# Kernel tuning notes

Hardware: AMD Instinct MI355X
Metric: run time of the kernel (lower is better)

## Reference

```python
import jax, jax.numpy as jnp
import numpy as np

L, C_IN, C, C_OUT, M, H, W = 4, 3, 64, 1, 64, 512, 512
INV_SQRT2 = 0.7071067811865476  # complex normal: re/im parts have variance 1/2


def setup_inputs() -> dict:
    key = jax.random.key(0)
    ks = jax.random.split(key, 12)

    def unif(k, shape, fan_in):
        lim = 1.0 / np.sqrt(fan_in)
        return jax.random.uniform(k, shape, jnp.float32, -lim, lim)

    return {
        "u": jax.random.normal(ks[0], (1, H, W), jnp.float32),
        "x": jax.random.normal(ks[1], (2, H, W), jnp.float32),
        "enc_w": unif(ks[2], (C, C_IN), C_IN),
        "enc_b": unif(ks[3], (C,), C_IN),
        "dec_w": unif(ks[4], (C_OUT, C), C),
        "dec_b": unif(ks[5], (C_OUT,), C),
        "conv1_w": unif(ks[6], (L, C, C), C),
        "conv1_b": unif(ks[7], (L, C), C),
        "conv2_w": unif(ks[8], (L, C, C), C),
        "conv2_b": unif(ks[9], (L, C), C),
        "A_re": jax.random.normal(ks[10], (L, C, C, M, M), jnp.float32) * INV_SQRT2,
        "A_im": jax.random.normal(ks[11], (L, C, C, M, M), jnp.float32) * INV_SQRT2,
    }


def pconv(w, b, v):
    # 1x1 conv == channel matmul: w [o,i], v [i,h,w]
    return jnp.einsum('oi,ihw->ohw', w, v) + b[:, None, None]


def spectral_conv(v, A):
    # v: [C, H, W] real; A: [C, C, M, M] complex
    Cv, Hv, Wv = v.shape
    c = jnp.fft.rfft2(v, norm='forward')[:, :, :M]      # truncate last axis -> [C, H, M]
    c = jnp.roll(c, M // 2, axis=1)[:, :M]              # center + truncate rows -> [C, M, M]
    c = jnp.einsum('oimn,imn->omn', A, c)               # per-mode channel mixing
    c = jnp.pad(c, ((0, 0), (0, Hv - M), (0, Wv // 2 + 1 - M)))
    c = jnp.roll(c, -(M // 2), axis=1)
    return jnp.fft.irfft2(c, s=(Hv, Wv), norm='forward')


def reference(u, x, enc_w, enc_b, dec_w, dec_b, conv1_w, conv1_b, conv2_w, conv2_b, A_re, A_im):
    A = A_re + 1j * A_im                                 # [L, C, C, M, M]
    v = jnp.concatenate([x, u], 0)                       # [C_IN, H, W]
    v = pconv(enc_w, enc_b, v)                           # [C, H, W]
    for l in range(A.shape[0]):
        s = spectral_conv(v, A[l])
        v = v + jax.nn.gelu(pconv(conv2_w[l], conv2_b[l], jax.nn.gelu(pconv(conv1_w[l], conv1_b[l], s))))
    return pconv(dec_w, dec_b, v)                        # [C_OUT, H, W]
```

## Files before the change

### kernel.cpp

```cpp
#include <hip/hip_runtime.h>


constexpr int Hn = 512, Wn = 512, Cn = 64, Mn = 64, Ln = 4;
constexpr int HWn = Hn * Wn;

typedef _Float16 half8 __attribute__((ext_vector_type(8)));
typedef float f32x4 __attribute__((ext_vector_type(4)));

__device__ __forceinline__ float gelu_f(float x) {
  float t = 0.7978845608028654f * (x + 0.044715f * x * x * x);
  float e = __expf(2.0f * t);
  float th = 1.0f - 2.0f / (e + 1.0f);
  return 0.5f * x * (1.0f + th);
}

__global__ __launch_bounds__(256) void k_init_tw(_Float16* __restrict__ B1t,
                                                 _Float16* __restrict__ A2t,
                                                 _Float16* __restrict__ A3t,
                                                 _Float16* __restrict__ B4t) {
  int j = blockIdx.x * 256 + threadIdx.x;
  const float TPI = 6.283185307179586f / 512.0f;
  {
    int n = j >> 9, w = j & 511;
    int idx = ((n & 63) * w) & 511;
    float ang = TPI * (float)idx;
    B1t[j] = (_Float16)((n < 64) ? cosf(ang) : -sinf(ang));
  }
  {
    int mp = j >> 9, h = j & 511;
    int idx = (((mp & 63) - 32) * h) & 511;
    float ang = TPI * (float)idx;
    A2t[j] = (_Float16)((mp < 64) ? cosf(ang) : -sinf(ang));
  }
  {
    int h = j >> 7, k = j & 127;
    int idx = (((k & 63) - 32) * h) & 511;
    float ang = TPI * (float)idx;
    A3t[j] = (_Float16)((k < 64) ? cosf(ang) : sinf(ang));
  }
  {
    int w = j >> 7, k = j & 127;
    int kk = k & 63;
    int idx = (kk * w) & 511;
    float ang = TPI * (float)idx;
    float al = (kk == 0) ? 1.0f : 2.0f;
    B4t[j] = (_Float16)((k < 64) ? al * cosf(ang) : -al * sinf(ang));
  }
}

__global__ __launch_bounds__(256) void k_encode(const float* __restrict__ u,
                                                const float* __restrict__ x,
                                                const float* __restrict__ ew,
                                                const float* __restrict__ eb,
                                                float* __restrict__ v) {
  __shared__ float w[Cn][3];
  __shared__ float b[Cn];
  int tid = threadIdx.x;
  if (tid < Cn) {
    w[tid][0] = ew[tid * 3 + 0];
    w[tid][1] = ew[tid * 3 + 1];
    w[tid][2] = ew[tid * 3 + 2];
    b[tid] = eb[tid];
  }
  __syncthreads();
  int p = blockIdx.x * 256 + tid;
  float x0 = x[p], x1 = x[HWn + p], uu = u[p];
  #pragma unroll 8
  for (int c = 0; c < Cn; c++)
    v[c * HWn + p] = fmaf(w[c][0], x0, fmaf(w[c][1], x1, fmaf(w[c][2], uu, b[c])));
}

__global__ __launch_bounds__(256) void k_fwd1(const float* __restrict__ v,
                                              const _Float16* __restrict__ B1t,
                                              _Float16* __restrict__ t1) {
  __shared__ _Float16 Vh[64 * 72];
  __shared__ _Float16 Bs[128 * 72];
  int tid = threadIdx.x;
  int wv = tid >> 6, lane = tid & 63;
  int col = lane & 15, quad = lane >> 4;
  int pb = blockIdx.x * 64;

  f32x4 acc[8];
  #pragma unroll
  for (int nt = 0; nt < 8; nt++) acc[nt] = (f32x4){0.f, 0.f, 0.f, 0.f};

  for (int kc = 0; kc < 8; kc++) {
    __syncthreads();
    #pragma unroll
    for (int i = 0; i < 4; i++) {
      int f = tid + 256 * i;
      int r_ = f >> 4, c4 = f & 15;
      float4 val = *(const float4*)&v[(size_t)(pb + r_) * Wn + kc * 64 + c4 * 4];
      union { _Float16 h4[4]; uint2 u; } pk;
      pk.h4[0] = (_Float16)val.x; pk.h4[1] = (_Float16)val.y;
      pk.h4[2] = (_Float16)val.z; pk.h4[3] = (_Float16)val.w;
      *(uint2*)&Vh[r_ * 72 + c4 * 4] = pk.u;
    }
    #pragma unroll
    for (int i = 0; i < 4; i++) {
      int f = tid + 256 * i;
      int r_ = f >> 3, c8 = f & 7;
      *(half8*)&Bs[r_ * 72 + c8 * 8] =
          *(const half8*)&B1t[r_ * 512 + kc * 64 + c8 * 8];
    }
    __syncthreads();
    #pragma unroll
    for (int kh = 0; kh < 2; kh++) {
      half8 a0 = *(const half8*)&Vh[(16 * wv + col) * 72 + kh * 32 + quad * 8];
      #pragma unroll
      for (int nt = 0; nt < 8; nt++) {
        half8 b = *(const half8*)&Bs[(nt * 16 + col) * 72 + kh * 32 + quad * 8];
        acc[nt] = __builtin_amdgcn_mfma_f32_16x16x32_f16(a0, b, acc[nt], 0, 0, 0);
      }
    }
  }
  int mrow = 16 * wv + quad * 4;
  int grow = pb + mrow;
  int ch = grow >> 9, h0 = grow & 511;
  #pragma unroll
  for (int nt = 0; nt < 8; nt++) {
    int ncol = nt * 16 + col;
    union { _Float16 h4[4]; uint2 u; } pk;
    #pragma unroll
    for (int r = 0; r < 4; r++) pk.h4[r] = (_Float16)acc[nt][r];
    *(uint2*)&t1[((size_t)ch * 128 + ncol) * 512 + h0] = pk.u;
  }
}

__global__ __launch_bounds__(256) void k_fwd2(const _Float16* __restrict__ t1,
                                              const _Float16* __restrict__ A2t,
                                              float2* __restrict__ cb) {
  __shared__ _Float16 Ash[128 * 72];
  __shared__ _Float16 Bsh[128 * 72];
  int tid = threadIdx.x;
  int wv = tid >> 6, lane = tid & 63;
  int col = lane & 15, quad = lane >> 4;
  int ch = blockIdx.x;

  f32x4 acc[2][8];
  #pragma unroll
  for (int mt = 0; mt < 2; mt++)
    #pragma unroll
    for (int nt = 0; nt < 8; nt++) acc[mt][nt] = (f32x4){0.f, 0.f, 0.f, 0.f};

  for (int kc = 0; kc < 8; kc++) {
    __syncthreads();
    #pragma unroll
    for (int i = 0; i < 4; i++) {
      int f = tid + 256 * i;
      int r_ = f >> 3, c8 = f & 7;
      *(half8*)&Ash[r_ * 72 + c8 * 8] =
          *(const half8*)&A2t[r_ * 512 + kc * 64 + c8 * 8];
      *(half8*)&Bsh[r_ * 72 + c8 * 8] =
          *(const half8*)&t1[((size_t)ch * 128 + r_) * 512 + kc * 64 + c8 * 8];
    }
    __syncthreads();
    #pragma unroll
    for (int kh = 0; kh < 2; kh++) {
      half8 a0 = *(const half8*)&Ash[(16 * wv + col) * 72 + kh * 32 + quad * 8];
      half8 a1 = *(const half8*)&Ash[(64 + 16 * wv + col) * 72 + kh * 32 + quad * 8];
      #pragma unroll
      for (int nt = 0; nt < 8; nt++) {
        half8 b = *(const half8*)&Bsh[(nt * 16 + col) * 72 + kh * 32 + quad * 8];
        acc[0][nt] = __builtin_amdgcn_mfma_f32_16x16x32_f16(a0, b, acc[0][nt], 0, 0, 0);
        acc[1][nt] = __builtin_amdgcn_mfma_f32_16x16x32_f16(a1, b, acc[1][nt], 0, 0, 0);
      }
    }
  }
  const float sc = 1.0f / 262144.0f;
  #pragma unroll
  for (int nt = 0; nt < 4; nt++) {
    #pragma unroll
    for (int r = 0; r < 4; r++) {
      int m = 16 * wv + quad * 4 + r;
      int n = 16 * nt + col;
      float cr = (acc[0][nt][r] - acc[1][nt + 4][r]) * sc;
      float ci = (acc[0][nt + 4][r] + acc[1][nt][r]) * sc;
      cb[((size_t)ch * 64 + m) * 64 + n] = make_float2(cr, ci);
    }
  }
}

__global__ __launch_bounds__(256) void k_mix(const float* __restrict__ Ar,
                                             const float* __restrict__ Ai,
                                             const float2* __restrict__ cb,
                                             float2* __restrict__ c2b) {
  __shared__ float2 csh[64][65];
  int tid = threadIdx.x;
  int m = blockIdx.x, og = blockIdx.y;
  for (int j = tid; j < 4096; j += 256) {
    int i = j >> 6, n = j & 63;
    csh[i][n] = cb[(i * 64 + m) * 64 + n];
  }
  __syncthreads();
  int o = og * 4 + (tid >> 6);
  int n = tid & 63;
  const float* ar = Ar + (size_t)o * 64 * 4096 + m * 64 + n;
  const float* ai = Ai + (size_t)o * 64 * 4096 + m * 64 + n;
  float accr = 0.f, acci = 0.f;
  #pragma unroll 8
  for (int i = 0; i < 64; i++) {
    float a_r = ar[i * 4096];
    float a_i = ai[i * 4096];
    float2 cv = csh[i][n];
    accr = fmaf(a_r, cv.x, fmaf(-a_i, cv.y, accr));
    acci = fmaf(a_r, cv.y, fmaf(a_i, cv.x, acci));
  }
  c2b[(o * 64 + m) * 64 + n] = make_float2(accr, acci);
}

__global__ __launch_bounds__(256) void k_inv1(const float2* __restrict__ c2,
                                              const _Float16* __restrict__ A3t,
                                              _Float16* __restrict__ e) {
  __shared__ _Float16 Csh[128 * 136];
  __shared__ _Float16 Hsh[128 * 136];
  int tid = threadIdx.x;
  int ch = blockIdx.x, hb = blockIdx.y;
  for (int j = tid; j < 4096; j += 256) {
    int m = j >> 6, n = j & 63;
    float2 cv = c2[(size_t)ch * 4096 + j];
    Csh[n * 136 + m]              = (_Float16)cv.x;
    Csh[(64 + n) * 136 + 64 + m]  = (_Float16)cv.x;
    Csh[(64 + n) * 136 + m]       = (_Float16)cv.y;
    Csh[n * 136 + 64 + m]         = (_Float16)(-cv.y);
  }
  #pragma unroll
  for (int i = 0; i < 8; i++) {
    int f = tid + 256 * i;
    int r_ = f >> 4, c8 = f & 15;
    *(half8*)&Hsh[r_ * 136 + c8 * 8] =
        *(const half8*)&A3t[(size_t)(hb * 128 + r_) * 128 + c8 * 8];
  }
  __syncthreads();
  int wv = tid >> 6, lane = tid & 63;
  int col = lane & 15, quad = lane >> 4;
  f32x4 acc[2][8];
  #pragma unroll
  for (int mt = 0; mt < 2; mt++)
    #pragma unroll
    for (int nt = 0; nt < 8; nt++) acc[mt][nt] = (f32x4){0.f, 0.f, 0.f, 0.f};
  #pragma unroll
  for (int ks = 0; ks < 4; ks++) {
    half8 a0 = *(const half8*)&Csh[(32 * wv + col) * 136 + ks * 32 + quad * 8];
    half8 a1 = *(const half8*)&Csh[(32 * wv + 16 + col) * 136 + ks * 32 + quad * 8];
    #pragma unroll
    for (int nt = 0; nt < 8; nt++) {
      half8 b = *(const half8*)&Hsh[(16 * nt + col) * 136 + ks * 32 + quad * 8];
      acc[0][nt] = __builtin_amdgcn_mfma_f32_16x16x32_f16(a0, b, acc[0][nt], 0, 0, 0);
      acc[1][nt] = __builtin_amdgcn_mfma_f32_16x16x32_f16(a1, b, acc[1][nt], 0, 0, 0);
    }
  }
  #pragma unroll
  for (int mt = 0; mt < 2; mt++) {
    int nn0 = 32 * wv + 16 * mt + quad * 4;
    #pragma unroll
    for (int nt = 0; nt < 8; nt++) {
      int h = hb * 128 + 16 * nt + col;
      union { _Float16 h4[4]; uint2 u; } pk;
      #pragma unroll
      for (int r = 0; r < 4; r++) pk.h4[r] = (_Float16)acc[mt][nt][r];
      *(uint2*)&e[((size_t)ch * 512 + h) * 128 + nn0] = pk.u;
    }
  }
}

__global__ __launch_bounds__(256) void k_inv2(const _Float16* __restrict__ e,
                                              const _Float16* __restrict__ B4t,
                                              _Float16* __restrict__ s) {
  __shared__ _Float16 Wsh[128 * 136];
  __shared__ _Float16 Esh[128 * 136];
  int tid = threadIdx.x;
  int pb = blockIdx.x * 128;
  int wb = blockIdx.y;
  #pragma unroll
  for (int i = 0; i < 8; i++) {
    int f = tid + 256 * i;
    int r_ = f >> 4, c8 = f & 15;
    *(half8*)&Wsh[r_ * 136 + c8 * 8] =
        *(const half8*)&B4t[(size_t)(wb * 128 + r_) * 128 + c8 * 8];
    *(half8*)&Esh[r_ * 136 + c8 * 8] =
        *(const half8*)&e[(size_t)(pb + r_) * 128 + c8 * 8];
  }
  __syncthreads();
  int wv = tid >> 6, lane = tid & 63;
  int col = lane & 15, quad = lane >> 4;
  f32x4 acc[2][8];
  #pragma unroll
  for (int mt = 0; mt < 2; mt++)
    #pragma unroll
    for (int nt = 0; nt < 8; nt++) acc[mt][nt] = (f32x4){0.f, 0.f, 0.f, 0.f};
  #pragma unroll
  for (int ks = 0; ks < 4; ks++) {
    half8 a0 = *(const half8*)&Wsh[(32 * wv + col) * 136 + ks * 32 + quad * 8];
    half8 a1 = *(const half8*)&Wsh[(32 * wv + 16 + col) * 136 + ks * 32 + quad * 8];
    #pragma unroll
    for (int nt = 0; nt < 8; nt++) {
      half8 b = *(const half8*)&Esh[(16 * nt + col) * 136 + ks * 32 + quad * 8];
      acc[0][nt] = __builtin_amdgcn_mfma_f32_16x16x32_f16(a0, b, acc[0][nt], 0, 0, 0);
      acc[1][nt] = __builtin_amdgcn_mfma_f32_16x16x32_f16(a1, b, acc[1][nt], 0, 0, 0);
    }
  }
  #pragma unroll
  for (int mt = 0; mt < 2; mt++) {
    int w0 = wb * 128 + 32 * wv + 16 * mt + quad * 4;
    #pragma unroll
    for (int nt = 0; nt < 8; nt++) {
      int prow = pb + 16 * nt + col;
      union { _Float16 h4[4]; uint2 u; } pk;
      #pragma unroll
      for (int r = 0; r < 4; r++) pk.h4[r] = (_Float16)acc[mt][nt][r];
      *(uint2*)&s[(size_t)prow * 512 + w0] = pk.u;
    }
  }
}

__global__ __launch_bounds__(256) void k_conv(const _Float16* __restrict__ s,
                                              float* __restrict__ v,
                                              const float* __restrict__ w1,
                                              const float* __restrict__ b1,
                                              const float* __restrict__ w2,
                                              const float* __restrict__ b2) {
  __shared__ _Float16 W1h[64 * 72];
  __shared__ _Float16 W2h[64 * 72];
  __shared__ _Float16 XpY2[64 * 72];
  __shared__ _Float16 Y1T[64 * 72];
  __shared__ float B1[64], B2[64];
  int tid = threadIdx.x;
  int pb = blockIdx.x * 64;

  for (int j = tid; j < 4096; j += 256) {
    int a_ = j >> 6, b_ = j & 63;
    W1h[a_ * 72 + b_] = (_Float16)w1[j];
    W2h[a_ * 72 + b_] = (_Float16)w2[j];
    XpY2[b_ * 72 + a_] = s[(size_t)a_ * HWn + pb + b_];
  }
  if (tid < 64) { B1[tid] = b1[tid]; B2[tid] = b2[tid]; }
  __syncthreads();

  int wv = tid >> 6, lane = tid & 63;
  int col = lane & 15, quad = lane >> 4;
  int prow = 16 * wv + col;

  f32x4 acc1[4];
  #pragma unroll
  for (int ot = 0; ot < 4; ot++) acc1[ot] = (f32x4){0.f, 0.f, 0.f, 0.f};
  half8 bfr[2];
  #pragma unroll
  for (int kh = 0; kh < 2; kh++)
    bfr[kh] = *(const half8*)&XpY2[prow * 72 + kh * 32 + quad * 8];
  #pragma unroll
  for (int ot = 0; ot < 4; ot++) {
    #pragma unroll
    for (int kh = 0; kh < 2; kh++) {
      half8 afr = *(const half8*)&W1h[(ot * 16 + col) * 72 + kh * 32 + quad * 8];
      acc1[ot] = __builtin_amdgcn_mfma_f32_16x16x32_f16(afr, bfr[kh], acc1[ot], 0, 0, 0);
    }
  }
  #pragma unroll
  for (int ot = 0; ot < 4; ot++) {
    int o0 = ot * 16 + quad * 4;
    union { _Float16 h[4]; uint2 u; } pk;
    #pragma unroll
    for (int r = 0; r < 4; r++)
      pk.h[r] = (_Float16)gelu_f(acc1[ot][r] + B1[o0 + r]);
    *(uint2*)&Y1T[prow * 72 + o0] = pk.u;
  }
  __syncthreads();

  f32x4 acc2[4];
  #pragma unroll
  for (int ot = 0; ot < 4; ot++) acc2[ot] = (f32x4){0.f, 0.f, 0.f, 0.f};
  #pragma unroll
  for (int kh = 0; kh < 2; kh++)
    bfr[kh] = *(const half8*)&Y1T[prow * 72 + kh * 32 + quad * 8];
  #pragma unroll
  for (int ot = 0; ot < 4; ot++) {
    #pragma unroll
    for (int kh = 0; kh < 2; kh++) {
      half8 afr = *(const half8*)&W2h[(ot * 16 + col) * 72 + kh * 32 + quad * 8];
      acc2[ot] = __builtin_amdgcn_mfma_f32_16x16x32_f16(afr, bfr[kh], acc2[ot], 0, 0, 0);
    }
  }
  #pragma unroll
  for (int ot = 0; ot < 4; ot++) {
    int o0 = ot * 16 + quad * 4;
    #pragma unroll
    for (int r = 0; r < 4; r++)
      XpY2[(o0 + r) * 66 + prow] = (_Float16)gelu_f(acc2[ot][r] + B2[o0 + r]);
  }
  __syncthreads();

  for (int j = tid; j < 4096; j += 256) {
    int o = j >> 6, p = j & 63;
    v[(size_t)o * HWn + pb + p] += (float)XpY2[o * 66 + p];
  }
}

__global__ __launch_bounds__(256) void k_decode(const float* __restrict__ v,
                                                const float* __restrict__ dw,
                                                const float* __restrict__ db,
                                                float* __restrict__ out) {
  __shared__ float wsm[64];
  int tid = threadIdx.x;
  if (tid < 64) wsm[tid] = dw[tid];
  __syncthreads();
  int p = blockIdx.x * 256 + tid;
  float acc = db[0];
  #pragma unroll
  for (int i = 0; i < 64; i++) acc = fmaf(wsm[i], v[i * HWn + p], acc);
  out[p] = acc;
}

extern "C" void kernel_launch(void* const* d_in, const int* in_sizes, int n_in,
                              void* d_out, int out_size, void* d_ws, size_t ws_size,
                              hipStream_t stream) {
  const float* u     = (const float*)d_in[0];
  const float* x     = (const float*)d_in[1];
  const float* enc_w = (const float*)d_in[2];
  const float* enc_b = (const float*)d_in[3];
  const float* dec_w = (const float*)d_in[4];
  const float* dec_b = (const float*)d_in[5];
  const float* c1w   = (const float*)d_in[6];
  const float* c1b   = (const float*)d_in[7];
  const float* c2w   = (const float*)d_in[8];
  const float* c2b   = (const float*)d_in[9];
  const float* Are   = (const float*)d_in[10];
  const float* Aim   = (const float*)d_in[11];
  float* out = (float*)d_out;
  float* ws = (float*)d_ws;

  _Float16* B1t = (_Float16*)ws;
  _Float16* A2t = B1t + 65536;
  _Float16* A3t = A2t + 65536;
  _Float16* B4t = A3t + 65536;
  float* v = ws + 131072;
  _Float16* sh = (_Float16*)(v + (size_t)Cn * HWn);
  _Float16* t1 = sh + (size_t)Cn * HWn;
  _Float16* e  = t1 + (size_t)Cn * 128 * 512;
  float2* cbuf = (float2*)(e + (size_t)Cn * 512 * 128);
  float2* cmix = cbuf + (size_t)Cn * Mn * Mn;

  k_init_tw<<<dim3(256), dim3(256), 0, stream>>>(B1t, A2t, A3t, B4t);
  k_encode<<<dim3(HWn / 256), dim3(256), 0, stream>>>(u, x, enc_w, enc_b, v);

  for (int l = 0; l < Ln; l++) {
    k_fwd1<<<dim3(Cn * Hn / 64), dim3(256), 0, stream>>>(v, B1t, t1);
    k_fwd2<<<dim3(Cn), dim3(256), 0, stream>>>(t1, A2t, cbuf);
    k_mix<<<dim3(Mn, 16), dim3(256), 0, stream>>>(
        Are + (size_t)l * Cn * Cn * Mn * Mn, Aim + (size_t)l * Cn * Cn * Mn * Mn,
        cbuf, cmix);
    k_inv1<<<dim3(Cn, 4), dim3(256), 0, stream>>>(cmix, A3t, e);
    k_inv2<<<dim3(Cn * Hn / 128, 4), dim3(256), 0, stream>>>(e, B4t, sh);
    k_conv<<<dim3(HWn / 64), dim3(256), 0, stream>>>(
        sh, v, c1w + (size_t)l * 4096, c1b + (size_t)l * 64,
        c2w + (size_t)l * 4096, c2b + (size_t)l * 64);
  }

  k_decode<<<dim3(HWn / 256), dim3(256), 0, stream>>>(v, dec_w, dec_b, out);

  (void)in_sizes; (void)n_in; (void)out_size; (void)ws_size;
}
```

Baseline: 972.3 us.

## Fuse inverse W-DFT, pointwise convs, residual and next forward DFT per row

Combines the inverse column DFT, the two 1x1 conv+GELU stages, the residual update, and the next layer's first forward DFT stage into one kernel that runs per image row. This removes the fp16 spatial intermediate and the separate fwd1 pass over v, cutting global memory traffic per layer. The t1 layout changes to [h][ch][128], so fwd2 now transposes through shared memory. k_inv1 is also retiled to 64-row blocks. The tail kernel launches only 512 blocks and uses more shared memory, which may limit occupancy.

```diff
diff --git a/kernel.cpp b/kernel.cpp
--- a/kernel.cpp
+++ b/kernel.cpp
@@ -73,16 +73,18 @@
 __global__ __launch_bounds__(256) void k_fwd1(const float* __restrict__ v,
                                               const _Float16* __restrict__ B1t,
                                               _Float16* __restrict__ t1) {
+  __shared__ _Float16 Ash[128 * 72];
   __shared__ _Float16 Vh[64 * 72];
-  __shared__ _Float16 Bs[128 * 72];
   int tid = threadIdx.x;
   int wv = tid >> 6, lane = tid & 63;
   int col = lane & 15, quad = lane >> 4;
   int pb = blockIdx.x * 64;
 
-  f32x4 acc[8];
-  #pragma unroll
-  for (int nt = 0; nt < 8; nt++) acc[nt] = (f32x4){0.f, 0.f, 0.f, 0.f};
+  f32x4 acc[2][4];
+  #pragma unroll
+  for (int mt = 0; mt < 2; mt++)
+    #pragma unroll
+    for (int nt = 0; nt < 4; nt++) acc[mt][nt] = (f32x4){0.f, 0.f, 0.f, 0.f};
 
   for (int kc = 0; kc < 8; kc++) {
     __syncthreads();
@@ -100,30 +102,34 @@
     for (int i = 0; i < 4; i++) {
       int f = tid + 256 * i;
       int r_ = f >> 3, c8 = f & 7;
-      *(half8*)&Bs[r_ * 72 + c8 * 8] =
-          *(const half8*)&B1t[r_ * 512 + kc * 64 + c8 * 8];
-    }
-    __syncthreads();
-    #pragma unroll
-    for (int kh = 0; kh < 2; kh++) {
-      half8 a0 = *(const half8*)&Vh[(16 * wv + col) * 72 + kh * 32 + quad * 8];
-      #pragma unroll
-      for (int nt = 0; nt < 8; nt++) {
-        half8 b = *(const half8*)&Bs[(nt * 16 + col) * 72 + kh * 32 + quad * 8];
-        acc[nt] = __builtin_amdgcn_mfma_f32_16x16x32_f16(a0, b, acc[nt], 0, 0, 0);
-      }
-    }
-  }
-  int mrow = 16 * wv + quad * 4;
-  int grow = pb + mrow;
-  int ch = grow >> 9, h0 = grow & 511;
-  #pragma unroll
-  for (int nt = 0; nt < 8; nt++) {
-    int ncol = nt * 16 + col;
-    union { _Float16 h4[4]; uint2 u; } pk;
-    #pragma unroll
-    for (int r = 0; r < 4; r++) pk.h4[r] = (_Float16)acc[nt][r];
-    *(uint2*)&t1[((size_t)ch * 128 + ncol) * 512 + h0] = pk.u;
+      *(half8*)&Ash[r_ * 72 + c8 * 8] =
+          *(const half8*)&B1t[(size_t)r_ * 512 + kc * 64 + c8 * 8];
+    }
+    __syncthreads();
+    #pragma unroll
+    for (int mt = 0; mt < 2; mt++)
+      #pragma unroll
+      for (int kh = 0; kh < 2; kh++) {
+        half8 af = *(const half8*)&Ash[(32 * wv + 16 * mt + col) * 72 + kh * 32 + quad * 8];
+        #pragma unroll
+        for (int nt = 0; nt < 4; nt++) {
+          half8 bf = *(const half8*)&Vh[(16 * nt + col) * 72 + kh * 32 + quad * 8];
+          acc[mt][nt] = __builtin_amdgcn_mfma_f32_16x16x32_f16(af, bf, acc[mt][nt], 0, 0, 0);
+        }
+      }
+  }
+  #pragma unroll
+  for (int mt = 0; mt < 2; mt++) {
+    int n0 = 32 * wv + 16 * mt + quad * 4;
+    #pragma unroll
+    for (int nt = 0; nt < 4; nt++) {
+      int prow = pb + 16 * nt + col;
+      int ch = prow >> 9, hh = prow & 511;
+      union { _Float16 h4[4]; uint2 u; } pk;
+      #pragma unroll
+      for (int r = 0; r < 4; r++) pk.h4[r] = (_Float16)acc[mt][nt][r];
+      *(uint2*)&t1[((size_t)hh * 64 + ch) * 128 + n0] = pk.u;
+    }
   }
 }
 
@@ -132,6 +138,7 @@
                                               float2* __restrict__ cb) {
   __shared__ _Float16 Ash[128 * 72];
   __shared__ _Float16 Bsh[128 * 72];
+  __shared__ _Float16 Tc[64 * 136];
   int tid = threadIdx.x;
   int wv = tid >> 6, lane = tid & 63;
   int col = lane & 15, quad = lane >> 4;
@@ -148,11 +155,23 @@
     #pragma unroll
     for (int i = 0; i < 4; i++) {
       int f = tid + 256 * i;
-      int r_ = f >> 3, c8 = f & 7;
-      *(half8*)&Ash[r_ * 72 + c8 * 8] =
-          *(const half8*)&A2t[r_ * 512 + kc * 64 + c8 * 8];
-      *(half8*)&Bsh[r_ * 72 + c8 * 8] =
-          *(const half8*)&t1[((size_t)ch * 128 + r_) * 512 + kc * 64 + c8 * 8];
+      {
+        int r_ = f >> 3, c8 = f & 7;
+        *(half8*)&Ash[r_ * 72 + c8 * 8] =
+            *(const half8*)&A2t[r_ * 512 + kc * 64 + c8 * 8];
+      }
+      {
+        int r_ = f >> 4, c8 = f & 15;
+        *(half8*)&Tc[r_ * 136 + c8 * 8] =
+            *(const half8*)&t1[((size_t)(kc * 64 + r_) * 64 + ch) * 128 + c8 * 8];
+      }
+    }
+    __syncthreads();
+    #pragma unroll 8
+    for (int i = 0; i < 32; i++) {
+      int f = tid + 256 * i;
+      int hh = f & 63, nn = f >> 6;
+      Bsh[nn * 72 + hh] = Tc[hh * 136 + nn];
     }
     __syncthreads();
     #pragma unroll
@@ -213,7 +232,7 @@
                                               const _Float16* __restrict__ A3t,
                                               _Float16* __restrict__ e) {
   __shared__ _Float16 Csh[128 * 136];
-  __shared__ _Float16 Hsh[128 * 136];
+  __shared__ _Float16 Hsh[64 * 136];
   int tid = threadIdx.x;
   int ch = blockIdx.x, hb = blockIdx.y;
   for (int j = tid; j < 4096; j += 256) {
@@ -225,26 +244,26 @@
     Csh[n * 136 + 64 + m]         = (_Float16)(-cv.y);
   }
   #pragma unroll
-  for (int i = 0; i < 8; i++) {
+  for (int i = 0; i < 4; i++) {
     int f = tid + 256 * i;
     int r_ = f >> 4, c8 = f & 15;
     *(half8*)&Hsh[r_ * 136 + c8 * 8] =
-        *(const half8*)&A3t[(size_t)(hb * 128 + r_) * 128 + c8 * 8];
+        *(const half8*)&A3t[(size_t)(hb * 64 + r_) * 128 + c8 * 8];
   }
   __syncthreads();
   int wv = tid >> 6, lane = tid & 63;
   int col = lane & 15, quad = lane >> 4;
-  f32x4 acc[2][8];
+  f32x4 acc[2][4];
   #pragma unroll
   for (int mt = 0; mt < 2; mt++)
     #pragma unroll
-    for (int nt = 0; nt < 8; nt++) acc[mt][nt] = (f32x4){0.f, 0.f, 0.f, 0.f};
+    for (int nt = 0; nt < 4; nt++) acc[mt][nt] = (f32x4){0.f, 0.f, 0.f, 0.f};
   #pragma unroll
   for (int ks = 0; ks < 4; ks++) {
     half8 a0 = *(const half8*)&Csh[(32 * wv + col) * 136 + ks * 32 + quad * 8];
     half8 a1 = *(const half8*)&Csh[(32 * wv + 16 + col) * 136 + ks * 32 + quad * 8];
     #pragma unroll
-    for (int nt = 0; nt < 8; nt++) {
+    for (int nt = 0; nt < 4; nt++) {
       half8 b = *(const half8*)&Hsh[(16 * nt + col) * 136 + ks * 32 + quad * 8];
       acc[0][nt] = __builtin_amdgcn_mfma_f32_16x16x32_f16(a0, b, acc[0][nt], 0, 0, 0);
       acc[1][nt] = __builtin_amdgcn_mfma_f32_16x16x32_f16(a1, b, acc[1][nt], 0, 0, 0);
@@ -254,8 +273,8 @@
   for (int mt = 0; mt < 2; mt++) {
     int nn0 = 32 * wv + 16 * mt + quad * 4;
     #pragma unroll
-    for (int nt = 0; nt < 8; nt++) {
-      int h = hb * 128 + 16 * nt + col;
+    for (int nt = 0; nt < 4; nt++) {
+      int h = hb * 64 + 16 * nt + col;
       union { _Float16 h4[4]; uint2 u; } pk;
       #pragma unroll
       for (int r = 0; r < 4; r++) pk.h4[r] = (_Float16)acc[mt][nt][r];
@@ -264,135 +283,181 @@
   }
 }
 
-__global__ __launch_bounds__(256) void k_inv2(const _Float16* __restrict__ e,
+template <bool WRITE_T1>
+__global__ __launch_bounds__(256) void k_tail(const _Float16* __restrict__ e,
+                                              float* __restrict__ v,
                                               const _Float16* __restrict__ B4t,
-                                              _Float16* __restrict__ s) {
-  __shared__ _Float16 Wsh[128 * 136];
-  __shared__ _Float16 Esh[128 * 136];
-  int tid = threadIdx.x;
-  int pb = blockIdx.x * 128;
-  int wb = blockIdx.y;
-  #pragma unroll
-  for (int i = 0; i < 8; i++) {
-    int f = tid + 256 * i;
-    int r_ = f >> 4, c8 = f & 15;
-    *(half8*)&Wsh[r_ * 136 + c8 * 8] =
-        *(const half8*)&B4t[(size_t)(wb * 128 + r_) * 128 + c8 * 8];
-    *(half8*)&Esh[r_ * 136 + c8 * 8] =
-        *(const half8*)&e[(size_t)(pb + r_) * 128 + c8 * 8];
-  }
-  __syncthreads();
-  int wv = tid >> 6, lane = tid & 63;
-  int col = lane & 15, quad = lane >> 4;
-  f32x4 acc[2][8];
-  #pragma unroll
-  for (int mt = 0; mt < 2; mt++)
-    #pragma unroll
-    for (int nt = 0; nt < 8; nt++) acc[mt][nt] = (f32x4){0.f, 0.f, 0.f, 0.f};
-  #pragma unroll
-  for (int ks = 0; ks < 4; ks++) {
-    half8 a0 = *(const half8*)&Wsh[(32 * wv + col) * 136 + ks * 32 + quad * 8];
-    half8 a1 = *(const half8*)&Wsh[(32 * wv + 16 + col) * 136 + ks * 32 + quad * 8];
-    #pragma unroll
-    for (int nt = 0; nt < 8; nt++) {
-      half8 b = *(const half8*)&Esh[(16 * nt + col) * 136 + ks * 32 + quad * 8];
-      acc[0][nt] = __builtin_amdgcn_mfma_f32_16x16x32_f16(a0, b, acc[0][nt], 0, 0, 0);
-      acc[1][nt] = __builtin_amdgcn_mfma_f32_16x16x32_f16(a1, b, acc[1][nt], 0, 0, 0);
-    }
-  }
-  #pragma unroll
-  for (int mt = 0; mt < 2; mt++) {
-    int w0 = wb * 128 + 32 * wv + 16 * mt + quad * 4;
-    #pragma unroll
-    for (int nt = 0; nt < 8; nt++) {
-      int prow = pb + 16 * nt + col;
-      union { _Float16 h4[4]; uint2 u; } pk;
-      #pragma unroll
-      for (int r = 0; r < 4; r++) pk.h4[r] = (_Float16)acc[mt][nt][r];
-      *(uint2*)&s[(size_t)prow * 512 + w0] = pk.u;
-    }
-  }
-}
-
-__global__ __launch_bounds__(256) void k_conv(const _Float16* __restrict__ s,
-                                              float* __restrict__ v,
+                                              const _Float16* __restrict__ B1t,
                                               const float* __restrict__ w1,
                                               const float* __restrict__ b1,
                                               const float* __restrict__ w2,
-                                              const float* __restrict__ b2) {
-  __shared__ _Float16 W1h[64 * 72];
-  __shared__ _Float16 W2h[64 * 72];
-  __shared__ _Float16 XpY2[64 * 72];
-  __shared__ _Float16 Y1T[64 * 72];
-  __shared__ float B1[64], B2[64];
-  int tid = threadIdx.x;
-  int pb = blockIdx.x * 64;
-
+                                              const float* __restrict__ b2,
+                                              _Float16* __restrict__ t1) {
+  __shared__ alignas(16) _Float16 E[64 * 136];
+  __shared__ alignas(16) _Float16 P[128 * 72];
+  __shared__ alignas(16) _Float16 XpVn[64 * 72];
+  __shared__ alignas(16) _Float16 Y1T[64 * 72];
+  __shared__ alignas(16) _Float16 W1h[64 * 72];
+  __shared__ alignas(16) _Float16 W2h[64 * 72];
+  __shared__ float B1s[64], B2s[64];
+  int tid = threadIdx.x;
+  int h = blockIdx.x;
+  int wv = tid >> 6, lane = tid & 63;
+  int col = lane & 15, quad = lane >> 4;
+  int prow = 16 * wv + col;
+
+  #pragma unroll
+  for (int i = 0; i < 4; i++) {
+    int f = tid + 256 * i;
+    int r_ = f >> 4, c8 = f & 15;
+    *(half8*)&E[r_ * 136 + c8 * 8] =
+        *(const half8*)&e[((size_t)r_ * 512 + h) * 128 + c8 * 8];
+  }
   for (int j = tid; j < 4096; j += 256) {
     int a_ = j >> 6, b_ = j & 63;
     W1h[a_ * 72 + b_] = (_Float16)w1[j];
     W2h[a_ * 72 + b_] = (_Float16)w2[j];
-    XpY2[b_ * 72 + a_] = s[(size_t)a_ * HWn + pb + b_];
-  }
-  if (tid < 64) { B1[tid] = b1[tid]; B2[tid] = b2[tid]; }
-  __syncthreads();
-
-  int wv = tid >> 6, lane = tid & 63;
-  int col = lane & 15, quad = lane >> 4;
-  int prow = 16 * wv + col;
-
-  f32x4 acc1[4];
-  #pragma unroll
-  for (int ot = 0; ot < 4; ot++) acc1[ot] = (f32x4){0.f, 0.f, 0.f, 0.f};
-  half8 bfr[2];
-  #pragma unroll
-  for (int kh = 0; kh < 2; kh++)
-    bfr[kh] = *(const half8*)&XpY2[prow * 72 + kh * 32 + quad * 8];
-  #pragma unroll
-  for (int ot = 0; ot < 4; ot++) {
-    #pragma unroll
-    for (int kh = 0; kh < 2; kh++) {
-      half8 afr = *(const half8*)&W1h[(ot * 16 + col) * 72 + kh * 32 + quad * 8];
-      acc1[ot] = __builtin_amdgcn_mfma_f32_16x16x32_f16(afr, bfr[kh], acc1[ot], 0, 0, 0);
-    }
-  }
-  #pragma unroll
-  for (int ot = 0; ot < 4; ot++) {
-    int o0 = ot * 16 + quad * 4;
-    union { _Float16 h[4]; uint2 u; } pk;
-    #pragma unroll
-    for (int r = 0; r < 4; r++)
-      pk.h[r] = (_Float16)gelu_f(acc1[ot][r] + B1[o0 + r]);
-    *(uint2*)&Y1T[prow * 72 + o0] = pk.u;
-  }
-  __syncthreads();
-
-  f32x4 acc2[4];
-  #pragma unroll
-  for (int ot = 0; ot < 4; ot++) acc2[ot] = (f32x4){0.f, 0.f, 0.f, 0.f};
-  #pragma unroll
-  for (int kh = 0; kh < 2; kh++)
-    bfr[kh] = *(const half8*)&Y1T[prow * 72 + kh * 32 + quad * 8];
-  #pragma unroll
-  for (int ot = 0; ot < 4; ot++) {
-    #pragma unroll
-    for (int kh = 0; kh < 2; kh++) {
-      half8 afr = *(const half8*)&W2h[(ot * 16 + col) * 72 + kh * 32 + quad * 8];
-      acc2[ot] = __builtin_amdgcn_mfma_f32_16x16x32_f16(afr, bfr[kh], acc2[ot], 0, 0, 0);
-    }
-  }
-  #pragma unroll
-  for (int ot = 0; ot < 4; ot++) {
-    int o0 = ot * 16 + quad * 4;
-    #pragma unroll
-    for (int r = 0; r < 4; r++)
-      XpY2[(o0 + r) * 66 + prow] = (_Float16)gelu_f(acc2[ot][r] + B2[o0 + r]);
-  }
-  __syncthreads();
-
-  for (int j = tid; j < 4096; j += 256) {
-    int o = j >> 6, p = j & 63;
-    v[(size_t)o * HWn + pb + p] += (float)XpY2[o * 66 + p];
+  }
+  if (tid < 64) { B1s[tid] = b1[tid]; B2s[tid] = b2[tid]; }
+
+  f32x4 acc2[2][4];
+  #pragma unroll
+  for (int mt = 0; mt < 2; mt++)
+    #pragma unroll
+    for (int nt = 0; nt < 4; nt++) acc2[mt][nt] = (f32x4){0.f, 0.f, 0.f, 0.f};
+
+  for (int wc = 0; wc < 8; wc++) {
+    int w0 = wc * 64;
+    __syncthreads();
+    #pragma unroll
+    for (int i = 0; i < 4; i++) {
+      int f = tid + 256 * i;
+      int r_ = f >> 4, c8 = f & 15;
+      *(half8*)&P[r_ * 136 + c8 * 8] =
+          *(const half8*)&B4t[(size_t)(w0 + r_) * 128 + c8 * 8];
+    }
+    __syncthreads();
+    {
+      f32x4 a0[4];
+      #pragma unroll
+      for (int nt = 0; nt < 4; nt++) a0[nt] = (f32x4){0.f, 0.f, 0.f, 0.f};
+      #pragma unroll
+      for (int ks = 0; ks < 4; ks++) {
+        half8 af = *(const half8*)&E[(16 * wv + col) * 136 + ks * 32 + quad * 8];
+        #pragma unroll
+        for (int nt = 0; nt < 4; nt++) {
+          half8 bf = *(const half8*)&P[(16 * nt + col) * 136 + ks * 32 + quad * 8];
+          a0[nt] = __builtin_amdgcn_mfma_f32_16x16x32_f16(af, bf, a0[nt], 0, 0, 0);
+        }
+      }
+      #pragma unroll
+      for (int nt = 0; nt < 4; nt++) {
+        union { _Float16 h4[4]; uint2 u; } pk;
+        #pragma unroll
+        for (int r = 0; r < 4; r++) pk.h4[r] = (_Float16)a0[nt][r];
+        *(uint2*)&XpVn[(16 * nt + col) * 72 + 16 * wv + quad * 4] = pk.u;
+      }
+    }
+    __syncthreads();
+    float* Vold = (float*)P;
+    #pragma unroll
+    for (int i = 0; i < 4; i++) {
+      int f = tid + 256 * i;
+      int r_ = f >> 4, c4 = f & 15;
+      *(f32x4*)&Vold[r_ * 68 + c4 * 4] =
+          *(const f32x4*)&v[(size_t)r_ * HWn + h * 512 + w0 + c4 * 4];
+    }
+    f32x4 a1[4];
+    #pragma unroll
+    for (int ot = 0; ot < 4; ot++) a1[ot] = (f32x4){0.f, 0.f, 0.f, 0.f};
+    {
+      half8 bfr[2];
+      #pragma unroll
+      for (int kh = 0; kh < 2; kh++)
+        bfr[kh] = *(const half8*)&XpVn[prow * 72 + kh * 32 + quad * 8];
+      #pragma unroll
+      for (int ot = 0; ot < 4; ot++) {
+        #pragma unroll
+        for (int kh = 0; kh < 2; kh++) {
+          half8 afr = *(const half8*)&W1h[(ot * 16 + col) * 72 + kh * 32 + quad * 8];
+          a1[ot] = __builtin_amdgcn_mfma_f32_16x16x32_f16(afr, bfr[kh], a1[ot], 0, 0, 0);
+        }
+      }
+      #pragma unroll
+      for (int ot = 0; ot < 4; ot++) {
+        int o0 = ot * 16 + quad * 4;
+        union { _Float16 h4[4]; uint2 u; } pk;
+        #pragma unroll
+        for (int r = 0; r < 4; r++)
+          pk.h4[r] = (_Float16)gelu_f(a1[ot][r] + B1s[o0 + r]);
+        *(uint2*)&Y1T[prow * 72 + o0] = pk.u;
+      }
+    }
+    __syncthreads();
+    {
+      f32x4 a2[4];
+      #pragma unroll
+      for (int ot = 0; ot < 4; ot++) a2[ot] = (f32x4){0.f, 0.f, 0.f, 0.f};
+      half8 bfr[2];
+      #pragma unroll
+      for (int kh = 0; kh < 2; kh++)
+        bfr[kh] = *(const half8*)&Y1T[prow * 72 + kh * 32 + quad * 8];
+      #pragma unroll
+      for (int ot = 0; ot < 4; ot++) {
+        #pragma unroll
+        for (int kh = 0; kh < 2; kh++) {
+          half8 afr = *(const half8*)&W2h[(ot * 16 + col) * 72 + kh * 32 + quad * 8];
+          a2[ot] = __builtin_amdgcn_mfma_f32_16x16x32_f16(afr, bfr[kh], a2[ot], 0, 0, 0);
+        }
+      }
+      #pragma unroll
+      for (int ot = 0; ot < 4; ot++) {
+        #pragma unroll
+        for (int r = 0; r < 4; r++) {
+          int ch = ot * 16 + quad * 4 + r;
+          float vo = Vold[ch * 68 + prow];
+          float vn = vo + gelu_f(a2[ot][r] + B2s[ch]);
+          v[(size_t)ch * HWn + h * 512 + w0 + prow] = vn;
+          XpVn[ch * 72 + prow] = (_Float16)vn;
+        }
+      }
+    }
+    __syncthreads();
+    if (WRITE_T1) {
+      #pragma unroll
+      for (int i = 0; i < 4; i++) {
+        int f = tid + 256 * i;
+        int r_ = f >> 3, c8 = f & 7;
+        *(half8*)&P[r_ * 72 + c8 * 8] =
+            *(const half8*)&B1t[(size_t)r_ * 512 + w0 + c8 * 8];
+      }
+      __syncthreads();
+      #pragma unroll
+      for (int mt = 0; mt < 2; mt++)
+        #pragma unroll
+        for (int kh = 0; kh < 2; kh++) {
+          half8 af = *(const half8*)&P[(32 * wv + 16 * mt + col) * 72 + kh * 32 + quad * 8];
+          #pragma unroll
+          for (int nt = 0; nt < 4; nt++) {
+            half8 bf = *(const half8*)&XpVn[(16 * nt + col) * 72 + kh * 32 + quad * 8];
+            acc2[mt][nt] = __builtin_amdgcn_mfma_f32_16x16x32_f16(af, bf, acc2[mt][nt], 0, 0, 0);
+          }
+        }
+    }
+  }
+  if (WRITE_T1) {
+    #pragma unroll
+    for (int mt = 0; mt < 2; mt++) {
+      int n0 = 32 * wv + 16 * mt + quad * 4;
+      #pragma unroll
+      for (int nt = 0; nt < 4; nt++) {
+        int ch = 16 * nt + col;
+        union { _Float16 h4[4]; uint2 u; } pk;
+        #pragma unroll
+        for (int r = 0; r < 4; r++) pk.h4[r] = (_Float16)acc2[mt][nt][r];
+        *(uint2*)&t1[((size_t)h * 64 + ch) * 128 + n0] = pk.u;
+      }
+    }
   }
 }
 
@@ -434,26 +499,30 @@
   _Float16* A3t = A2t + 65536;
   _Float16* B4t = A3t + 65536;
   float* v = ws + 131072;
-  _Float16* sh = (_Float16*)(v + (size_t)Cn * HWn);
-  _Float16* t1 = sh + (size_t)Cn * HWn;
-  _Float16* e  = t1 + (size_t)Cn * 128 * 512;
-  float2* cbuf = (float2*)(e + (size_t)Cn * 512 * 128);
+  _Float16* t1 = (_Float16*)(v + (size_t)Cn * HWn);
+  _Float16* e  = t1 + (size_t)Hn * Cn * 128;
+  float2* cbuf = (float2*)(e + (size_t)Cn * Hn * 128);
   float2* cmix = cbuf + (size_t)Cn * Mn * Mn;
 
   k_init_tw<<<dim3(256), dim3(256), 0, stream>>>(B1t, A2t, A3t, B4t);
   k_encode<<<dim3(HWn / 256), dim3(256), 0, stream>>>(u, x, enc_w, enc_b, v);
+  k_fwd1<<<dim3(Cn * Hn / 64), dim3(256), 0, stream>>>(v, B1t, t1);
 
   for (int l = 0; l < Ln; l++) {
-    k_fwd1<<<dim3(Cn * Hn / 64), dim3(256), 0, stream>>>(v, B1t, t1);
     k_fwd2<<<dim3(Cn), dim3(256), 0, stream>>>(t1, A2t, cbuf);
     k_mix<<<dim3(Mn, 16), dim3(256), 0, stream>>>(
         Are + (size_t)l * Cn * Cn * Mn * Mn, Aim + (size_t)l * Cn * Cn * Mn * Mn,
         cbuf, cmix);
-    k_inv1<<<dim3(Cn, 4), dim3(256), 0, stream>>>(cmix, A3t, e);
-    k_inv2<<<dim3(Cn * Hn / 128, 4), dim3(256), 0, stream>>>(e, B4t, sh);
-    k_conv<<<dim3(HWn / 64), dim3(256), 0, stream>>>(
-        sh, v, c1w + (size_t)l * 4096, c1b + (size_t)l * 64,
-        c2w + (size_t)l * 4096, c2b + (size_t)l * 64);
+    k_inv1<<<dim3(Cn, 8), dim3(256), 0, stream>>>(cmix, A3t, e);
+    if (l < Ln - 1) {
+      k_tail<true><<<dim3(Hn), dim3(256), 0, stream>>>(
+          e, v, B4t, B1t, c1w + (size_t)l * 4096, c1b + (size_t)l * 64,
+          c2w + (size_t)l * 4096, c2b + (size_t)l * 64, t1);
+    } else {
+      k_tail<false><<<dim3(Hn), dim3(256), 0, stream>>>(
+          e, v, B4t, B1t, c1w + (size_t)l * 4096, c1b + (size_t)l * 64,
+          c2w + (size_t)l * 4096, c2b + (size_t)l * 64, t1);
+    }
   }
 
   k_decode<<<dim3(HWn / 256), dim3(256), 0, stream>>>(v, dec_w, dec_b, out);
```

Measured after the change: 970.7 us. Within noise of the previous version (-0.2%).
